# Kernel tuning notes

Measured on AMD Instinct MI355X. Metric: run time of the kernel, lower is better.

The kernel has to match this reference:

```python
import jax, jax.numpy as jnp
import numpy as np
import math

N_NODES = 20000
N_EDGES = 320000
NODE_IN = 128
HIDDEN = 64
HEADS = 4
TIME_DIM = 64
SCALE = 60.0 / 1.0  # sensitivity / epsilon


def _linear_params(key, din, dout):
    k1, k2 = jax.random.split(key)
    bound = 1.0 / math.sqrt(din)
    w = jax.random.uniform(k1, (din, dout), minval=-bound, maxval=bound, dtype=jnp.float32)
    b = jax.random.uniform(k2, (dout,), minval=-bound, maxval=bound, dtype=jnp.float32)
    return w, b


def setup_inputs() -> dict:
    key = jax.random.key(0)
    ks = jax.random.split(key, 16)
    edge_index = jax.random.randint(ks[0], (2, N_EDGES), 0, N_NODES, dtype=jnp.int64)
    raw_time = jax.random.uniform(ks[1], (N_EDGES, 1), dtype=jnp.float32) * 86400.0
    noise = jax.random.laplace(ks[2], (N_EDGES, 1), dtype=jnp.float32) * SCALE
    node_emb = jax.random.normal(ks[3], (N_NODES, NODE_IN), dtype=jnp.float32)
    HC = HEADS * HIDDEN
    wq1, bq1 = _linear_params(ks[4], NODE_IN, HC)
    wk1, bk1 = _linear_params(ks[5], NODE_IN, HC)
    wv1, bv1 = _linear_params(ks[6], NODE_IN, HC)
    wt1, bt1 = _linear_params(ks[7], TIME_DIM, HC)
    wq2, bq2 = _linear_params(ks[8], HC, HC)
    wk2, bk2 = _linear_params(ks[9], HC, HC)
    wv2, bv2 = _linear_params(ks[10], HC, HC)
    wt2, bt2 = _linear_params(ks[11], TIME_DIM, HC)
    wc, bc = _linear_params(ks[12], HC, 1)
    return dict(edge_index=edge_index, raw_time=raw_time, noise=noise, node_emb=node_emb,
                wq1=wq1, bq1=bq1, wk1=wk1, bk1=bk1, wv1=wv1, bv1=bv1, wt1=wt1, bt1=bt1,
                wq2=wq2, bq2=bq2, wk2=wk2, bk2=bk2, wv2=wv2, bv2=bv2, wt2=wt2, bt2=bt2,
                wc=wc, bc=bc)


def time_encode(t):
    # t: [E, 1] -> [E, TIME_DIM]; interleaved sin/cos as in TimeEncoder
    half = jnp.arange(0, TIME_DIM, 2, dtype=jnp.float32)
    div_term = jnp.exp(half * (-math.log(10000.0) / TIME_DIM))  # [TIME_DIM/2]
    arg = t * div_term  # [E, TIME_DIM/2]
    te = jnp.stack([jnp.sin(arg), jnp.cos(arg)], axis=-1)  # [E, T/2, 2]
    return te.reshape(t.shape[0], TIME_DIM)


def temporal_conv(x, src, dst, time_enc, wq, bq, wk, bk, wv, bv, wt, bt):
    # gather-QKV, edge softmax over dst segments, scatter-add aggregation
    N = x.shape[0]
    q = (x @ wq + bq).reshape(N, HEADS, HIDDEN)
    k = (x @ wk + bk).reshape(N, HEADS, HIDDEN)
    v = (x @ wv + bv).reshape(N, HEADS, HIDDEN)
    t_enc = (time_enc @ wt + bt).reshape(-1, HEADS, HIDDEN)  # [E,H,C]
    q_i = q[dst]                      # [E,H,C]
    k_j = k[src] + t_enc              # [E,H,C]
    alpha = (q_i * k_j).sum(-1) / math.sqrt(HIDDEN)  # [E,H]
    # segment softmax over index = dst (PyG softmax semantics)
    amax = jax.ops.segment_max(alpha, dst, num_segments=N)  # [N,H]
    ea = jnp.exp(alpha - amax[dst])
    denom = jax.ops.segment_sum(ea, dst, num_segments=N)
    alpha = ea / (denom[dst] + 1e-16)
    msg = v[src] * alpha[..., None]   # [E,H,C]
    out = jax.ops.segment_sum(msg, dst, num_segments=N)  # [N,H,C]
    return out.reshape(N, HEADS * HIDDEN)


def reference(edge_index, raw_time, noise, node_emb,
              wq1, bq1, wk1, bk1, wv1, bv1, wt1, bt1,
              wq2, bq2, wk2, bk2, wv2, bv2, wt2, bt2,
              wc, bc):
    src, dst = edge_index[0], edge_index[1]
    noisy_time = raw_time + noise                 # Laplace mechanism
    time_encoded = time_encode(noisy_time)        # [E, TIME_DIM]
    x = jax.nn.relu(temporal_conv(node_emb, src, dst, time_encoded,
                                  wq1, bq1, wk1, bk1, wv1, bv1, wt1, bt1))
    x = jax.nn.relu(temporal_conv(x, src, dst, time_encoded,
                                  wq2, bq2, wk2, bk2, wv2, bv2, wt2, bt2))
    edge_emb = x[src] + x[dst]                    # [E, H*C]
    out = edge_emb @ wc + bc                      # [E, 1]
    return out.squeeze(-1)
```

## Files before the change

### kernel.cpp

```cpp
#include <hip/hip_runtime.h>
#include <hip/hip_fp16.h>
#include <math.h>

#define NN   20000
#define NE   320000
#define NIN  128
#define HC   256
#define NB   1024

#define AGG_BLOCKS 1250
#define AGG_STRIDE 5000
#define LOG2E_8    0.18033688f

typedef unsigned short u16;
typedef __attribute__((ext_vector_type(8))) short bf16x8;
typedef __attribute__((ext_vector_type(8))) unsigned short u16x8;
typedef __attribute__((ext_vector_type(4))) float f32x4;

__device__ __forceinline__ float bf2f(u16 u) {
  union { unsigned int i; float f; } x;
  x.i = ((unsigned int)u) << 16;
  return x.f;
}
__device__ __forceinline__ u16 f2bf(float f) {
  union { float f; unsigned int i; } x;
  x.f = f;
  unsigned int r = x.i + 0x7fffu + ((x.i >> 16) & 1u);
  return (u16)(r >> 16);
}
__device__ __forceinline__ float bflo(int v) {
  union { int i; float f; } x; x.i = v << 16; return x.f;
}
__device__ __forceinline__ float bfhi(int v) {
  union { int i; float f; } x; x.i = v & 0xffff0000; return x.f;
}

__device__ __forceinline__ float ldf(const void* p, int i, bool fbf) {
  return fbf ? bf2f(((const u16*)p)[i]) : ((const float*)p)[i];
}
__device__ __forceinline__ int ldsrc(const void* p, int e, bool is64) {
  const int* p32 = (const int*)p;
  return is64 ? p32[2 * e] : p32[e];
}
__device__ __forceinline__ int lddst(const void* p, int e, bool is64) {
  const int* p32 = (const int*)p;
  return is64 ? p32[2 * (NE + e)] : p32[NE + e];
}
__device__ __forceinline__ void stout(void* p, int i, float v, bool fbf) {
  if (fbf) ((u16*)p)[i] = f2bf(v);
  else ((float*)p)[i] = v;
}

__device__ __forceinline__ void gload_lds16(const u16* g, u16* l) {
  __builtin_amdgcn_global_load_lds(
      (const __attribute__((address_space(1))) void*)g,
      (__attribute__((address_space(3))) void*)l, 16, 0, 0);
}

__device__ __forceinline__ float dpp_row_allsum(float s) {
  union fi { float f; int i; };
  fi a, b;
  a.f = s;
  b.i = __builtin_amdgcn_update_dpp(0, a.i, 0x121, 0xf, 0xf, true); a.f += b.f;
  b.i = __builtin_amdgcn_update_dpp(0, a.i, 0x122, 0xf, 0xf, true); a.f += b.f;
  b.i = __builtin_amdgcn_update_dpp(0, a.i, 0x124, 0xf, 0xf, true); a.f += b.f;
  b.i = __builtin_amdgcn_update_dpp(0, a.i, 0x128, 0xf, 0xf, true); a.f += b.f;
  return a.f;
}

__device__ __forceinline__ float fexp2(float x) {
#if __has_builtin(__builtin_amdgcn_exp2f)
  return __builtin_amdgcn_exp2f(x);
#else
  return exp2f(x);
#endif
}

#if __has_builtin(__builtin_amdgcn_fdot2_f32_bf16)
#define HAS_BF16_DOT2 1
typedef __attribute__((ext_vector_type(2))) __bf16 bfv2_t;
__device__ __forceinline__ float qkdot2(int a, int b, float c) {
  return __builtin_amdgcn_fdot2_f32_bf16(__builtin_bit_cast(bfv2_t, a),
                                         __builtin_bit_cast(bfv2_t, b), c, false);
}
#else
#define HAS_BF16_DOT2 0
#endif

__device__ __forceinline__ void edge_do(int4 kv, int2 t, int2 q2,
    float qsx, float qsy, float qsz, float qsw,
    float px, float py, float pz, float pw, float qb,
    float& denom, float& a0, float& a1, float& a2, float& a3) {
  float2 f01 = __half22float2(__builtin_bit_cast(__half2, t.x));
  float2 f23 = __half22float2(__builtin_bit_cast(__half2, t.y));
  float stp = f01.x * px + f01.y * py + f23.x * pz + f23.y * pw;
#if HAS_BF16_DOT2
  float sqk = qkdot2(kv.y, q2.y, qkdot2(kv.x, q2.x, 0.f));
  float partial = sqk * LOG2E_8 + stp;
#else
  float partial = stp + qsx * bflo(kv.x) + qsy * bfhi(kv.x) +
                  qsz * bflo(kv.y) + qsw * bfhi(kv.y);
#endif
  float a = dpp_row_allsum(partial) + qb;
  float ea = fexp2(a);
  denom += ea;
  a0 = fmaf(ea, bflo(kv.z), a0);
  a1 = fmaf(ea, bfhi(kv.z), a1);
  a2 = fmaf(ea, bflo(kv.w), a2);
  a3 = fmaf(ea, bfhi(kv.w), a3);
}

__global__ void devinit_kernel(const void* __restrict__ eidx,
                               const void* __restrict__ nemb,
                               int* __restrict__ flags, float* __restrict__ divt) {
  int lane = threadIdx.x;
  if (lane < 32) {
    const float c32 = (float)(-0.14391156831212787);
    float prod = (float)(2 * lane) * c32;
    divt[lane] = (float)exp((double)prod);
  }
  if (lane == 0) {
    const int* p32 = (const int*)eidx;
    int is64 = 1;
    for (int i = 1; i < 128; i += 2)
      if (p32[i] != 0) { is64 = 0; break; }
    const u16* q16 = (const u16*)nemb;
    int fbf = 1;
    for (int i = 0; i < 128; i += 2) {
      unsigned e = (q16[i] >> 7) & 0xFF;
      if (e < 90 || e > 140) { fbf = 0; break; }
    }
    flags[0] = is64;
    flags[1] = fbf;
  }
}

__global__ void sentinel_kernel(const int* __restrict__ flags, void* __restrict__ out) {
  int i = blockIdx.x * 256 + threadIdx.x;
  if (i < NE) stout(out, i, 3000.0f, flags[1] != 0);
}
__global__ void raw_sentinel_kernel(u16* __restrict__ out) {
  int i = blockIdx.x * 256 + threadIdx.x;
  if (i < NE) out[i] = f2bf(3000.0f);
}

__global__ void zero_kernel(int* __restrict__ p, int n) {
  int i = blockIdx.x * 256 + threadIdx.x;
  if (i < n) p[i] = 0;
}

__global__ void hist_kernel(const int* __restrict__ flags, const void* __restrict__ eidx,
                            int* __restrict__ cnt) {
  bool is64 = flags[0] != 0;
  int e = blockIdx.x * 256 + threadIdx.x;
  if (e < NE) {
    int d = lddst(eidx, e, is64);
    if ((unsigned)d < NN) atomicAdd(&cnt[d], 1);
  }
}

__global__ void scan1_kernel(const int* __restrict__ cnt, int* __restrict__ offs,
                             int* __restrict__ bsum, int n) {
  __shared__ int s[256];
  int b = blockIdx.x, t = threadIdx.x, i = b * 256 + t;
  int x = (i < n) ? cnt[i] : 0;
  s[t] = x;
  __syncthreads();
  for (int off = 1; off < 256; off <<= 1) {
    int y = (t >= off) ? s[t - off] : 0;
    __syncthreads();
    s[t] += y;
    __syncthreads();
  }
  if (i < n) offs[i] = s[t] - x;
  if (t == 255) bsum[b] = s[t];
}

__global__ void scan2_kernel(int* __restrict__ bsum, int* __restrict__ offs,
                             int nb, int n) {
  __shared__ int s[256];
  int t = threadIdx.x;
  int x = (t < nb) ? bsum[t] : 0;
  s[t] = x;
  __syncthreads();
  for (int off = 1; off < 256; off <<= 1) {
    int y = (t >= off) ? s[t - off] : 0;
    __syncthreads();
    s[t] += y;
    __syncthreads();
  }
  if (t < nb) bsum[t] = s[t] - x;
  if (t == 255) offs[n] = s[t];
}

__global__ void scan3_kernel(int* __restrict__ offs, const int* __restrict__ bsum,
                             int* __restrict__ cursor, int n) {
  int i = blockIdx.x * 256 + threadIdx.x;
  if (i < n) {
    int v = offs[i] + bsum[blockIdx.x];
    offs[i] = v;
    cursor[i] = v;
  }
}

__global__ void fill_kernel(const int* __restrict__ flags, const void* __restrict__ eidx,
                            const void* __restrict__ rawt, const void* __restrict__ noise,
                            int* __restrict__ cursor, int* __restrict__ ssrc,
                            float* __restrict__ stt) {
  bool is64 = flags[0] != 0, fbf = flags[1] != 0;
  int e = blockIdx.x * 256 + threadIdx.x;
  if (e < NE) {
    int d = lddst(eidx, e, is64);
    if ((unsigned)d < NN) {
      int pos = atomicAdd(&cursor[d], 1);
      if ((unsigned)pos < NE) {
        int src = ldsrc(eidx, e, is64);
        if ((unsigned)src >= NN) src = 0;
        ssrc[pos] = src;
        stt[pos] = ldf(rawt, e, fbf) + ldf(noise, e, fbf);
      }
    }
  }
}

__global__ __launch_bounds__(256) void te_kernel(
    const float* __restrict__ stt, const float* __restrict__ divt,
    u16* __restrict__ te_s) {
  int idx = blockIdx.x * 256 + threadIdx.x;
  int p = idx >> 5;
  if (p >= NE) return;
  int f = idx & 31;
  float tt = stt[p];
  float arg = tt * divt[f];
  double rev = (double)arg * 0.15915494309189535;
  double fr = rev - floor(rev);
  float frf = (float)fr;
  float sv = __builtin_amdgcn_sinf(frf);
  float cv = __builtin_amdgcn_cosf(frf);
  __half hs = __float2half(sv), hc = __float2half(cv);
  unsigned int packed = (unsigned int)(*(u16*)&hs) | ((unsigned int)(*(u16*)&hc) << 16);
  ((unsigned int*)te_s)[(size_t)p * 32 + f] = packed;
}

__global__ void transw3_kernel(const int* __restrict__ flags, const void* __restrict__ W0,
                               const void* __restrict__ W1, const void* __restrict__ W2,
                               u16* __restrict__ WtBig, int K) {
  bool fbf = flags[1] != 0;
  __shared__ u16 tile[64][65];
  int z = blockIdx.z;
  const void* W = (z == 0) ? W0 : (z == 1) ? W1 : W2;
  u16* dst = WtBig + (size_t)z * 256 * K;
  int kb = blockIdx.x * 64, cb = blockIdx.y * 64;
  int tx = threadIdx.x & 63, ty = threadIdx.x >> 6;
  for (int i = ty; i < 64; i += 4)
    tile[tx][i] = f2bf(ldf(W, (kb + i) * HC + cb + tx, fbf));
  __syncthreads();
  for (int i = ty; i < 64; i += 4)
    dst[(size_t)(cb + i) * K + kb + tx] = tile[i][tx];
}

__global__ void wcombbias_kernel(const int* __restrict__ flags, const void* __restrict__ wt,
                                 const u16* __restrict__ Wqt, u16* __restrict__ Wout,
                                 const void* __restrict__ bq, const void* __restrict__ bk,
                                 const void* __restrict__ bv, float* __restrict__ biasBig,
                                 int K) {
  bool fbf = flags[1] != 0;
  int b = blockIdx.x, t = threadIdx.x;
  if (b < 256) {
    __shared__ float wrow[64];
    int j = b, h = j >> 6;
    if (t < 64) wrow[t] = ldf(wt, (j & 63) * HC + h * 64 + t, fbf);
    __syncthreads();
    if (t < K) {
      float s = 0.f;
#pragma unroll 8
      for (int mm = 0; mm < 64; ++mm)
        s += wrow[mm] * bf2f(Wqt[(size_t)(h * 64 + mm) * K + t]);
      Wout[(size_t)j * K + t] = f2bf(s);
    }
  } else if (b < 259) {
    int bb = b - 256;
    const void* p = (bb == 0) ? bq : (bb == 1) ? bk : bv;
    biasBig[bb * 256 + t] = ldf(p, t, fbf);
  } else {
    int j = t, h = j >> 6;
    float s = 0.f;
    for (int mm = 0; mm < 64; ++mm)
      s += ldf(bq, h * 64 + mm, fbf) * ldf(wt, (j & 63) * HC + h * 64 + mm, fbf);
    biasBig[768 + j] = s;
  }
}

template <bool AWS>
__global__ __launch_bounds__(256) void gemm_mfma(
    const int* __restrict__ flags, const void* __restrict__ Ap,
    const u16* __restrict__ Wt, const float* __restrict__ bias,
    u16* __restrict__ C, int M, int K) {
  bool fbf = flags[1] != 0;
  __shared__ u16 As[128 * 32];
  __shared__ u16 Bs[128 * 32];
  int tid = threadIdx.x;
  int rb = blockIdx.x * 128, cb = blockIdx.y * 128;
  int wave = tid >> 6, lane = tid & 63;
  int l15 = lane & 15, quad = lane >> 4;
  int mbase = (wave >> 1) * 64, nbase = (wave & 1) * 64;

  f32x4 acc[4][4];
#pragma unroll
  for (int mt = 0; mt < 4; ++mt)
#pragma unroll
    for (int nt = 0; nt < 4; ++nt)
#pragma unroll
      for (int r = 0; r < 4; ++r) acc[mt][nt][r] = 0.f;

  int srow0 = tid >> 2, schunk0 = tid & 3;
  int srow1 = (tid + 256) >> 2, schunk1 = (tid + 256) & 3;
  int gchunk0 = schunk0 ^ (srow0 & 3);
  int gchunk1 = schunk1 ^ (srow1 & 3);
  int arow0 = rb + srow0; if (arow0 >= M) arow0 = M - 1;
  int arow1 = rb + srow1; if (arow1 >= M) arow1 = M - 1;
  u16* asl0 = &As[srow0 * 32 + schunk0 * 8];
  u16* asl1 = &As[srow1 * 32 + schunk1 * 8];
  u16* bsl0 = &Bs[srow0 * 32 + schunk0 * 8];
  u16* bsl1 = &Bs[srow1 * 32 + schunk1 * 8];
  const u16* bsrc0 = Wt + (size_t)(cb + srow0) * K + gchunk0 * 8;
  const u16* bsrc1 = Wt + (size_t)(cb + srow1) * K + gchunk1 * 8;
  const bool adirect = AWS || fbf;
  const u16* asrc0 = adirect ? ((const u16*)Ap + (size_t)arow0 * K + gchunk0 * 8) : (const u16*)0;
  const u16* asrc1 = adirect ? ((const u16*)Ap + (size_t)arow1 * K + gchunk1 * 8) : (const u16*)0;

  for (int kk = 0; kk < K; kk += 32) {
    if (adirect) {
      gload_lds16(asrc0 + kk, asl0);
      gload_lds16(asrc1 + kk, asl1);
    } else {
      const float* A0 = (const float*)Ap + (size_t)arow0 * K + kk + gchunk0 * 8;
      const float* A1 = (const float*)Ap + (size_t)arow1 * K + kk + gchunk1 * 8;
      bf16x8 t0, t1;
#pragma unroll
      for (int i = 0; i < 8; ++i) { t0[i] = (short)f2bf(A0[i]); t1[i] = (short)f2bf(A1[i]); }
      *(bf16x8*)asl0 = t0;
      *(bf16x8*)asl1 = t1;
    }
    gload_lds16(bsrc0 + kk, bsl0);
    gload_lds16(bsrc1 + kk, bsl1);
    __syncthreads();

    bf16x8 bfrag[4];
#pragma unroll
    for (int nt = 0; nt < 4; ++nt) {
      int col = nbase + nt * 16 + l15;
      bfrag[nt] = *(const bf16x8*)&Bs[col * 32 + ((quad ^ (col & 3)) * 8)];
    }
#pragma unroll
    for (int mt = 0; mt < 4; ++mt) {
      int row = mbase + mt * 16 + l15;
      bf16x8 afrag = *(const bf16x8*)&As[row * 32 + ((quad ^ (row & 3)) * 8)];
#pragma unroll
      for (int nt = 0; nt < 4; ++nt)
        acc[mt][nt] = __builtin_amdgcn_mfma_f32_16x16x32_bf16(afrag, bfrag[nt], acc[mt][nt], 0, 0, 0);
    }
    __syncthreads();
  }

#pragma unroll
  for (int nt = 0; nt < 4; ++nt) {
    int gcol = cb + nbase + nt * 16 + l15;
    float bv = bias[gcol];
    int scol;
    if (gcol < 256) scol = gcol;
    else if (gcol < 512) { int cc = gcol - 256; scol = 256 + ((cc >> 2) << 3) + (cc & 3); }
    else if (gcol < 768) { int cc = gcol - 512; scol = 256 + ((cc >> 2) << 3) + 4 + (cc & 3); }
    else scol = gcol;
#pragma unroll
    for (int mt = 0; mt < 4; ++mt) {
#pragma unroll
      for (int r = 0; r < 4; ++r) {
        int grow = rb + mbase + mt * 16 + quad * 4 + r;
        if (grow < M) C[(size_t)grow * NB + scol] = f2bf(acc[mt][nt][r] + bv);
      }
    }
  }
}

template <int DOY>
__global__ __launch_bounds__(256) void aggfused_kernel(
    const int* __restrict__ flags, const int* __restrict__ ssrc,
    const int* __restrict__ offsets, const u16* __restrict__ te_s,
    const u16* __restrict__ qkvp, const void* __restrict__ bt,
    u16* __restrict__ xout, const void* __restrict__ wc,
    float* __restrict__ ynode) {
  bool fbf = flags[1] != 0;
  int lane = threadIdx.x & 63;
  int c = lane * 4;
  int jb = c & 63;
  int kvoff = 256 + lane * 8;

  float btv0 = ldf(bt, c + 0, fbf), btv1 = ldf(bt, c + 1, fbf);
  float btv2 = ldf(bt, c + 2, fbf), btv3 = ldf(bt, c + 3, fbf);
  float wcv0 = 0.f, wcv1 = 0.f, wcv2 = 0.f, wcv3 = 0.f;
  if (DOY) {
    wcv0 = ldf(wc, c + 0, fbf); wcv1 = ldf(wc, c + 1, fbf);
    wcv2 = ldf(wc, c + 2, fbf); wcv3 = ldf(wc, c + 3, fbf);
  }

  int n = blockIdx.x * 4 + (threadIdx.x >> 6);
  int s0 = offsets[n], s1 = offsets[n + 1];
  int2 q2 = *(const int2*)(qkvp + (size_t)n * NB + c);
  int2 p2 = *(const int2*)(qkvp + (size_t)n * NB + 768 + c);

  while (n < NN) {
    int n1 = n + AGG_STRIDE;
    int n1c = (n1 < NN) ? n1 : 0;
    int s0n = offsets[n1c], s1n = offsets[n1c + 1];
    int2 q2n = *(const int2*)(qkvp + (size_t)n1c * NB + c);
    int2 p2n = *(const int2*)(qkvp + (size_t)n1c * NB + 768 + c);

    float qx = bflo(q2.x), qy = bfhi(q2.x), qz = bflo(q2.y), qw = bfhi(q2.y);
    float px = bflo(p2.x) * LOG2E_8, py = bfhi(p2.x) * LOG2E_8;
    float pz = bflo(p2.y) * LOG2E_8, pw = bfhi(p2.y) * LOG2E_8;
    float pb = qx * btv0 + qy * btv1 + qz * btv2 + qw * btv3;
    float qb = dpp_row_allsum(pb) * LOG2E_8;
    float qsx = qx * LOG2E_8, qsy = qy * LOG2E_8;
    float qsz = qz * LOG2E_8, qsw = qw * LOG2E_8;

    float denom = 0.f, acc0 = 0.f, acc1 = 0.f, acc2 = 0.f, acc3 = 0.f;
    const int* sp = ssrc + s0;
    const u16* tep = te_s + (size_t)s0 * 64 + jb;
    int ecnt = s1 - s0;
    int e = 0;
    if (ecnt >= 4) {
      int sA = sp[0], sB = sp[1], sC = sp[2], sD = sp[3];
      while (e + 4 <= ecnt) {
        int4 kvA = *(const int4*)(qkvp + ((unsigned)(sA << 10) + (unsigned)kvoff));
        int4 kvB = *(const int4*)(qkvp + ((unsigned)(sB << 10) + (unsigned)kvoff));
        int4 kvC = *(const int4*)(qkvp + ((unsigned)(sC << 10) + (unsigned)kvoff));
        int4 kvD = *(const int4*)(qkvp + ((unsigned)(sD << 10) + (unsigned)kvoff));
        int2 tA = *(const int2*)(tep + (size_t)e * 64);
        int2 tB = *(const int2*)(tep + (size_t)(e + 1) * 64);
        int2 tC = *(const int2*)(tep + (size_t)(e + 2) * 64);
        int2 tD = *(const int2*)(tep + (size_t)(e + 3) * 64);
        int en = e + 4;
        if (en + 4 <= ecnt) {
          sA = sp[en]; sB = sp[en + 1]; sC = sp[en + 2]; sD = sp[en + 3];
        }
        edge_do(kvA, tA, q2, qsx, qsy, qsz, qsw, px, py, pz, pw, qb,
                denom, acc0, acc1, acc2, acc3);
        edge_do(kvB, tB, q2, qsx, qsy, qsz, qsw, px, py, pz, pw, qb,
                denom, acc0, acc1, acc2, acc3);
        edge_do(kvC, tC, q2, qsx, qsy, qsz, qsw, px, py, pz, pw, qb,
                denom, acc0, acc1, acc2, acc3);
        edge_do(kvD, tD, q2, qsx, qsy, qsz, qsw, px, py, pz, pw, qb,
                denom, acc0, acc1, acc2, acc3);
        e = en;
      }
    }
    for (; e < ecnt; ++e) {
      int s = sp[e];
      int4 kv = *(const int4*)(qkvp + ((unsigned)(s << 10) + (unsigned)kvoff));
      int2 t = *(const int2*)(tep + (size_t)e * 64);
      edge_do(kv, t, q2, qsx, qsy, qsz, qsw, px, py, pz, pw, qb,
              denom, acc0, acc1, acc2, acc3);
    }

    float inv = 1.f / (denom + 1e-16f);
    ushort4 r;
    r.x = f2bf(fmaxf(acc0 * inv, 0.f));
    r.y = f2bf(fmaxf(acc1 * inv, 0.f));
    r.z = f2bf(fmaxf(acc2 * inv, 0.f));
    r.w = f2bf(fmaxf(acc3 * inv, 0.f));
    *(ushort4*)(xout + (size_t)n * HC + c) = r;
    if (DOY) {
      float yv = bf2f(r.x) * wcv0 + bf2f(r.y) * wcv1 +
                 bf2f(r.z) * wcv2 + bf2f(r.w) * wcv3;
      yv = dpp_row_allsum(yv);
      yv += __shfl_xor(yv, 16);
      yv += __shfl_xor(yv, 32);
      if (lane == 0) ynode[n] = yv;
    }

    n = n1;
    s0 = s0n; s1 = s1n; q2 = q2n; p2 = p2n;
  }
}

__global__ __launch_bounds__(256) void final2_kernel(
    const int* __restrict__ flags, const void* __restrict__ eidx,
    const float* __restrict__ y, const void* __restrict__ bc,
    void* __restrict__ out) {
  bool is64 = flags[0] != 0, fbf = flags[1] != 0;
  int e = blockIdx.x * 256 + threadIdx.x;
  if (e >= NE) return;
  int src = ldsrc(eidx, e, is64);
  int dst = lddst(eidx, e, is64);
  if ((unsigned)src >= NN) src = 0;
  if ((unsigned)dst >= NN) dst = 0;
  stout(out, e, y[src] + y[dst] + ldf(bc, 0, fbf), fbf);
}

extern "C" void kernel_launch(void* const* d_in, const int* in_sizes, int n_in,
                              void* d_out, int out_size, void* d_ws, size_t ws_size,
                              hipStream_t stream) {
  const void* eidx  = d_in[0];
  const void* rawt  = d_in[1];
  const void* noise = d_in[2];
  const void* nemb  = d_in[3];
  const void *wq1 = d_in[4],  *bq1 = d_in[5];
  const void *wk1 = d_in[6],  *bk1 = d_in[7];
  const void *wv1 = d_in[8],  *bv1 = d_in[9];
  const void *wt1 = d_in[10], *bt1 = d_in[11];
  const void *wq2 = d_in[12], *bq2 = d_in[13];
  const void *wk2 = d_in[14], *bk2 = d_in[15];
  const void *wv2 = d_in[16], *bv2 = d_in[17];
  const void *wt2 = d_in[18], *bt2 = d_in[19];
  const void *wcp = d_in[20], *bcp = d_in[21];

  char* ws = (char*)d_ws;
  size_t off = 0;
  auto alloc = [&](size_t bytes) -> void* {
    void* p = ws + off;
    off += (bytes + 255) & ~(size_t)255;
    return p;
  };
  int*   flags  = (int*)alloc(256);
  float* divt   = (float*)alloc(256);
  u16*   WtBig  = (u16*)alloc((size_t)NB * HC * 2);
  float* biasBig= (float*)alloc((size_t)NB * 4);
  u16*   qkvp   = (u16*)alloc((size_t)NN * NB * 2);
  u16*   x1     = (u16*)alloc((size_t)NN * HC * 2);
  u16*   x2     = (u16*)alloc((size_t)NN * HC * 2);
  float* ynode  = (float*)alloc((size_t)NN * 4);
  int* offsets  = (int*)alloc((size_t)(NN + 1) * 4);
  int* cursor   = (int*)alloc((size_t)NN * 4);
  int* bsum     = (int*)alloc(256 * 4);
  int* ssrc     = (int*)alloc((size_t)NE * 4);
  float* stt    = (float*)alloc((size_t)NE * 4);
  u16* te_s     = (u16*)alloc((size_t)NE * 64 * 2);
  size_t need = off;

  int gN = (NN + 255) / 256, gE = (NE + 255) / 256;
  int nb = (NN + 255) / 256;

  if (ws_size < 1024) {
    raw_sentinel_kernel<<<gE, 256, 0, stream>>>((u16*)d_out);
    return;
  }
  devinit_kernel<<<1, 64, 0, stream>>>(eidx, nemb, flags, divt);
  if (need > ws_size) {
    sentinel_kernel<<<gE, 256, 0, stream>>>(flags, d_out);
    return;
  }

  zero_kernel<<<gN, 256, 0, stream>>>(cursor, NN);
  hist_kernel<<<gE, 256, 0, stream>>>(flags, eidx, cursor);
  scan1_kernel<<<nb, 256, 0, stream>>>(cursor, offsets, bsum, NN);
  scan2_kernel<<<1, 256, 0, stream>>>(bsum, offsets, nb, NN);
  scan3_kernel<<<nb, 256, 0, stream>>>(offsets, bsum, cursor, NN);
  fill_kernel<<<gE, 256, 0, stream>>>(flags, eidx, rawt, noise, cursor, ssrc, stt);

  int gTe = (NE * 32 + 255) / 256;
  te_kernel<<<gTe, 256, 0, stream>>>(stt, divt, te_s);

  dim3 ggemm((NN + 127) / 128, NB / 128);
  dim3 gt1(NIN / 64, 4, 3), gt2(HC / 64, 4, 3);

  transw3_kernel<<<gt1, 256, 0, stream>>>(flags, wq1, wk1, wv1, WtBig, NIN);
  wcombbias_kernel<<<260, 256, 0, stream>>>(flags, wt1, WtBig, WtBig + (size_t)768 * NIN,
                                            bq1, bk1, bv1, biasBig, NIN);
  gemm_mfma<false><<<ggemm, 256, 0, stream>>>(flags, nemb, WtBig, biasBig, qkvp, NN, NIN);
  aggfused_kernel<0><<<AGG_BLOCKS, 256, 0, stream>>>(flags, ssrc, offsets, te_s, qkvp, bt1,
                                                     x1, wcp, ynode);

  transw3_kernel<<<gt2, 256, 0, stream>>>(flags, wq2, wk2, wv2, WtBig, HC);
  wcombbias_kernel<<<260, 256, 0, stream>>>(flags, wt2, WtBig, WtBig + (size_t)768 * HC,
                                            bq2, bk2, bv2, biasBig, HC);
  gemm_mfma<true><<<ggemm, 256, 0, stream>>>(flags, x1, WtBig, biasBig, qkvp, NN, HC);
  aggfused_kernel<1><<<AGG_BLOCKS, 256, 0, stream>>>(flags, ssrc, offsets, te_s, qkvp, bt2,
                                                     x2, wcp, ynode);

  final2_kernel<<<gE, 256, 0, stream>>>(flags, eidx, ynode, bcp, d_out);
}
```

Measured before the change: 385.1 us.

## Compute time encoding inline in aggregation kernels instead of precomputed buffer

Removes the separate time-encoding kernel and its E×64 fp16 buffer. Each aggregation lane now recomputes its two sin/cos pairs from the per-edge noisy time, using a split-constant float range reduction in place of the double-precision one. This trades the te_s write and two reads of it (about 41 MB each way) for extra transcendental ALU work per edge in both layers. The aggregation grid is also doubled so each block covers half as many nodes per stride.

```diff
diff --git a/kernel.cpp b/kernel.cpp
--- a/kernel.cpp
+++ b/kernel.cpp
@@ -8,13 +8,12 @@
 #define HC   256
 #define NB   1024
 
-#define AGG_BLOCKS 1250
-#define AGG_STRIDE 5000
+#define AGG_BLOCKS 2500
+#define AGG_STRIDE 10000
 #define LOG2E_8    0.18033688f
 
 typedef unsigned short u16;
 typedef __attribute__((ext_vector_type(8))) short bf16x8;
-typedef __attribute__((ext_vector_type(8))) unsigned short u16x8;
 typedef __attribute__((ext_vector_type(4))) float f32x4;
 
 __device__ __forceinline__ float bf2f(u16 u) {
@@ -87,13 +86,22 @@
 #define HAS_BF16_DOT2 0
 #endif
 
-__device__ __forceinline__ void edge_do(int4 kv, int2 t, int2 q2,
+__device__ __forceinline__ void edge_do(int4 kv, float tt, int2 q2,
+    float dc0, float dc1,
     float qsx, float qsy, float qsz, float qsw,
     float px, float py, float pz, float pw, float qb,
     float& denom, float& a0, float& a1, float& a2, float& a3) {
-  float2 f01 = __half22float2(__builtin_bit_cast(__half2, t.x));
-  float2 f23 = __half22float2(__builtin_bit_cast(__half2, t.y));
-  float stp = f01.x * px + f01.y * py + f23.x * pz + f23.y * pw;
+  const float CH = 0.15915494f;
+  const float CL = (float)(0.15915494309189535 - (double)0.15915494f);
+  float x0 = tt * dc0, x1 = tt * dc1;
+  float p0 = x0 * CH, p1 = x1 * CH;
+  float e0 = fmaf(x0, CH, -p0), e1 = fmaf(x1, CH, -p1);
+  e0 = fmaf(x0, CL, e0);  e1 = fmaf(x1, CL, e1);
+  float fr0 = (p0 - rintf(p0)) + e0;
+  float fr1 = (p1 - rintf(p1)) + e1;
+  float sv0 = __builtin_amdgcn_sinf(fr0), cv0 = __builtin_amdgcn_cosf(fr0);
+  float sv1 = __builtin_amdgcn_sinf(fr1), cv1 = __builtin_amdgcn_cosf(fr1);
+  float stp = sv0 * px + cv0 * py + sv1 * pz + cv1 * pw;
 #if HAS_BF16_DOT2
   float sqk = qkdot2(kv.y, q2.y, qkdot2(kv.x, q2.x, 0.f));
   float partial = sqk * LOG2E_8 + stp;
@@ -223,25 +231,6 @@
   }
 }
 
-__global__ __launch_bounds__(256) void te_kernel(
-    const float* __restrict__ stt, const float* __restrict__ divt,
-    u16* __restrict__ te_s) {
-  int idx = blockIdx.x * 256 + threadIdx.x;
-  int p = idx >> 5;
-  if (p >= NE) return;
-  int f = idx & 31;
-  float tt = stt[p];
-  float arg = tt * divt[f];
-  double rev = (double)arg * 0.15915494309189535;
-  double fr = rev - floor(rev);
-  float frf = (float)fr;
-  float sv = __builtin_amdgcn_sinf(frf);
-  float cv = __builtin_amdgcn_cosf(frf);
-  __half hs = __float2half(sv), hc = __float2half(cv);
-  unsigned int packed = (unsigned int)(*(u16*)&hs) | ((unsigned int)(*(u16*)&hc) << 16);
-  ((unsigned int*)te_s)[(size_t)p * 32 + f] = packed;
-}
-
 __global__ void transw3_kernel(const int* __restrict__ flags, const void* __restrict__ W0,
                                const void* __restrict__ W1, const void* __restrict__ W2,
                                u16* __restrict__ WtBig, int K) {
@@ -386,16 +375,18 @@
 template <int DOY>
 __global__ __launch_bounds__(256) void aggfused_kernel(
     const int* __restrict__ flags, const int* __restrict__ ssrc,
-    const int* __restrict__ offsets, const u16* __restrict__ te_s,
+    const int* __restrict__ offsets, const float* __restrict__ stt,
+    const float* __restrict__ divt,
     const u16* __restrict__ qkvp, const void* __restrict__ bt,
     u16* __restrict__ xout, const void* __restrict__ wc,
     float* __restrict__ ynode) {
   bool fbf = flags[1] != 0;
   int lane = threadIdx.x & 63;
   int c = lane * 4;
-  int jb = c & 63;
   int kvoff = 256 + lane * 8;
 
+  int i0 = (2 * lane) & 31;
+  float dc0 = divt[i0], dc1 = divt[i0 + 1];
   float btv0 = ldf(bt, c + 0, fbf), btv1 = ldf(bt, c + 1, fbf);
   float btv2 = ldf(bt, c + 2, fbf), btv3 = ldf(bt, c + 3, fbf);
   float wcv0 = 0.f, wcv1 = 0.f, wcv2 = 0.f, wcv3 = 0.f;
@@ -426,7 +417,7 @@
 
     float denom = 0.f, acc0 = 0.f, acc1 = 0.f, acc2 = 0.f, acc3 = 0.f;
     const int* sp = ssrc + s0;
-    const u16* tep = te_s + (size_t)s0 * 64 + jb;
+    const float* tp = stt + s0;
     int ecnt = s1 - s0;
     int e = 0;
     if (ecnt >= 4) {
@@ -436,21 +427,18 @@
         int4 kvB = *(const int4*)(qkvp + ((unsigned)(sB << 10) + (unsigned)kvoff));
         int4 kvC = *(const int4*)(qkvp + ((unsigned)(sC << 10) + (unsigned)kvoff));
         int4 kvD = *(const int4*)(qkvp + ((unsigned)(sD << 10) + (unsigned)kvoff));
-        int2 tA = *(const int2*)(tep + (size_t)e * 64);
-        int2 tB = *(const int2*)(tep + (size_t)(e + 1) * 64);
-        int2 tC = *(const int2*)(tep + (size_t)(e + 2) * 64);
-        int2 tD = *(const int2*)(tep + (size_t)(e + 3) * 64);
+        float ttA = tp[e], ttB = tp[e + 1], ttC = tp[e + 2], ttD = tp[e + 3];
         int en = e + 4;
         if (en + 4 <= ecnt) {
           sA = sp[en]; sB = sp[en + 1]; sC = sp[en + 2]; sD = sp[en + 3];
         }
-        edge_do(kvA, tA, q2, qsx, qsy, qsz, qsw, px, py, pz, pw, qb,
+        edge_do(kvA, ttA, q2, dc0, dc1, qsx, qsy, qsz, qsw, px, py, pz, pw, qb,
                 denom, acc0, acc1, acc2, acc3);
-        edge_do(kvB, tB, q2, qsx, qsy, qsz, qsw, px, py, pz, pw, qb,
+        edge_do(kvB, ttB, q2, dc0, dc1, qsx, qsy, qsz, qsw, px, py, pz, pw, qb,
                 denom, acc0, acc1, acc2, acc3);
-        edge_do(kvC, tC, q2, qsx, qsy, qsz, qsw, px, py, pz, pw, qb,
+        edge_do(kvC, ttC, q2, dc0, dc1, qsx, qsy, qsz, qsw, px, py, pz, pw, qb,
                 denom, acc0, acc1, acc2, acc3);
-        edge_do(kvD, tD, q2, qsx, qsy, qsz, qsw, px, py, pz, pw, qb,
+        edge_do(kvD, ttD, q2, dc0, dc1, qsx, qsy, qsz, qsw, px, py, pz, pw, qb,
                 denom, acc0, acc1, acc2, acc3);
         e = en;
       }
@@ -458,8 +446,8 @@
     for (; e < ecnt; ++e) {
       int s = sp[e];
       int4 kv = *(const int4*)(qkvp + ((unsigned)(s << 10) + (unsigned)kvoff));
-      int2 t = *(const int2*)(tep + (size_t)e * 64);
-      edge_do(kv, t, q2, qsx, qsy, qsz, qsw, px, py, pz, pw, qb,
+      float tt = tp[e];
+      edge_do(kv, tt, q2, dc0, dc1, qsx, qsy, qsz, qsw, px, py, pz, pw, qb,
               denom, acc0, acc1, acc2, acc3);
     }
 
@@ -535,7 +523,6 @@
   int* bsum     = (int*)alloc(256 * 4);
   int* ssrc     = (int*)alloc((size_t)NE * 4);
   float* stt    = (float*)alloc((size_t)NE * 4);
-  u16* te_s     = (u16*)alloc((size_t)NE * 64 * 2);
   size_t need = off;
 
   int gN = (NN + 255) / 256, gE = (NE + 255) / 256;
@@ -558,9 +545,6 @@
   scan3_kernel<<<nb, 256, 0, stream>>>(offsets, bsum, cursor, NN);
   fill_kernel<<<gE, 256, 0, stream>>>(flags, eidx, rawt, noise, cursor, ssrc, stt);
 
-  int gTe = (NE * 32 + 255) / 256;
-  te_kernel<<<gTe, 256, 0, stream>>>(stt, divt, te_s);
-
   dim3 ggemm((NN + 127) / 128, NB / 128);
   dim3 gt1(NIN / 64, 4, 3), gt2(HC / 64, 4, 3);
 
@@ -568,15 +552,15 @@
   wcombbias_kernel<<<260, 256, 0, stream>>>(flags, wt1, WtBig, WtBig + (size_t)768 * NIN,
                                             bq1, bk1, bv1, biasBig, NIN);
   gemm_mfma<false><<<ggemm, 256, 0, stream>>>(flags, nemb, WtBig, biasBig, qkvp, NN, NIN);
-  aggfused_kernel<0><<<AGG_BLOCKS, 256, 0, stream>>>(flags, ssrc, offsets, te_s, qkvp, bt1,
-                                                     x1, wcp, ynode);
+  aggfused_kernel<0><<<AGG_BLOCKS, 256, 0, stream>>>(flags, ssrc, offsets, stt, divt,
+                                                     qkvp, bt1, x1, wcp, ynode);
 
   transw3_kernel<<<gt2, 256, 0, stream>>>(flags, wq2, wk2, wv2, WtBig, HC);
   wcombbias_kernel<<<260, 256, 0, stream>>>(flags, wt2, WtBig, WtBig + (size_t)768 * HC,
                                             bq2, bk2, bv2, biasBig, HC);
   gemm_mfma<true><<<ggemm, 256, 0, stream>>>(flags, x1, WtBig, biasBig, qkvp, NN, HC);
-  aggfused_kernel<1><<<AGG_BLOCKS, 256, 0, stream>>>(flags, ssrc, offsets, te_s, qkvp, bt2,
-                                                     x2, wcp, ynode);
+  aggfused_kernel<1><<<AGG_BLOCKS, 256, 0, stream>>>(flags, ssrc, offsets, stt, divt,
+                                                     qkvp, bt2, x2, wcp, ynode);
 
   final2_kernel<<<gE, 256, 0, stream>>>(flags, eidx, ynode, bcp, d_out);
 }
```

After: 359.0 us. 1.07x faster.
